# Optimization experiments

Hardware: AMD Instinct MI355X
Metric: run time of the kernel (lower is better)

Reference implementation:

```python
import jax, jax.numpy as jnp
import numpy as np

B, N_Q, N_K, DIM = 4, 4096, 4096, 256
INNER = 64
N_TOPK = 3
MINUS_INF = -1e9


def setup_inputs() -> dict:
    key = jax.random.key(0)
    ks = jax.random.split(key, 5)
    q = jax.random.normal(ks[0], (B, N_Q, DIM), dtype=jnp.float32)
    k = jax.random.normal(ks[1], (B, N_K, DIM), dtype=jnp.float32)
    v = jax.random.normal(ks[2], (B, N_K, DIM), dtype=jnp.float32)
    Wq = jax.random.normal(ks[3], (DIM, INNER), dtype=jnp.float32) * 0.02
    Wk = jax.random.normal(ks[4], (DIM, INNER), dtype=jnp.float32) * 0.02
    return {"q": q, "k": k, "v": v, "Wq": Wq, "Wk": Wk}


def reference(q, k, v, Wq, Wk):
    # v is accepted but unused, matching the torch module.
    scale = INNER ** (-0.5)  # dim_head == inner_dim == 64
    qh = (q @ Wq) * scale            # [B, N_Q, 64]
    kh = k @ Wk                      # [B, N_K, 64]
    # heads = 1 -> scores [B, 1, N_Q, N_K]
    scores = jnp.einsum('bqd,bkd->bqk', qh, kh)[:, None]
    # torch.kthvalue(k=N_K - 3) == 4th-largest value per row
    thresh = jax.lax.top_k(scores, N_TOPK + 1)[0][..., N_TOPK:N_TOPK + 1]
    masked = jnp.where(scores < thresh, MINUS_INF, scores)
    return jax.nn.softmax(masked, axis=-1)
```

## Files before the change

kernel.cpp:

```cpp
#include <hip/hip_runtime.h>
#include <hip/hip_bf16.h>
#include <math.h>

typedef float v4f __attribute__((ext_vector_type(4)));
typedef short bf16x8 __attribute__((ext_vector_type(8)));
typedef float f32x16 __attribute__((ext_vector_type(16)));

#define BATCH 4
#define NQ 4096
#define NK 4096
#define DIM 256
#define INNER 64
#define NEG_INF (-3.0e38f)
#define CAP 64

__global__ __launch_bounds__(256) void proj_kernel(
    const float* __restrict__ q, const float* __restrict__ k,
    const float* __restrict__ Wq, const float* __restrict__ Wk,
    float* __restrict__ qh, float* __restrict__ kh,
    ushort* __restrict__ qhb, ushort* __restrict__ khb)
{
  __shared__ float xs[32 * 260];
  const int bid = blockIdx.x;
  const bool isq = bid < 512;
  const float* X   = isq ? q : k;
  const float* W   = isq ? Wq : Wk;
  float*   out     = isq ? qh : kh;
  const float scale = isq ? 0.125f : 1.0f;
  const int row0 = (isq ? bid : bid - 512) * 32;
  const int t = threadIdx.x;

  #pragma unroll
  for (int it = 0; it < 8; ++it) {
    int idx = it * 256 + t;
    int r = idx >> 6, dq = idx & 63;
    v4f v = *reinterpret_cast<const v4f*>(X + (size_t)(row0 + r) * DIM + dq * 4);
    *reinterpret_cast<v4f*>(&xs[r * 260 + dq * 4]) = v;
  }
  __syncthreads();

  const int i0 = (t & 15) * 4;
  const int rg = t >> 4;
  float acc[2][4];
  #pragma unroll
  for (int p = 0; p < 2; ++p)
    #pragma unroll
    for (int i = 0; i < 4; ++i) acc[p][i] = 0.f;

  for (int d0 = 0; d0 < DIM; d0 += 4) {
    v4f w0 = *reinterpret_cast<const v4f*>(W + (d0 + 0) * INNER + i0);
    v4f w1 = *reinterpret_cast<const v4f*>(W + (d0 + 1) * INNER + i0);
    v4f w2 = *reinterpret_cast<const v4f*>(W + (d0 + 2) * INNER + i0);
    v4f w3 = *reinterpret_cast<const v4f*>(W + (d0 + 3) * INNER + i0);
    #pragma unroll
    for (int p = 0; p < 2; ++p) {
      v4f x = *reinterpret_cast<const v4f*>(&xs[(rg + 16 * p) * 260 + d0]);
      #pragma unroll
      for (int i = 0; i < 4; ++i) {
        float bs = x[0] * w0[i];
        bs = fmaf(x[1], w1[i], bs);
        bs = fmaf(x[2], w2[i], bs);
        bs = fmaf(x[3], w3[i], bs);
        acc[p][i] += bs;
      }
    }
  }

  const int d  = i0 >> 4;
  const int hi = (i0 >> 3) & 1;
  const int e0 = i0 & 7;
  #pragma unroll
  for (int p = 0; p < 2; ++p) {
    v4f o;
    ushort ob[4];
    #pragma unroll
    for (int i = 0; i < 4; ++i) {
      o[i] = acc[p][i] * scale;
      __hip_bfloat16 h = __float2bfloat16(o[i]);
      ob[i] = *reinterpret_cast<ushort*>(&h);
    }
    int rr = rg + 16 * p;
    size_t row = (size_t)(row0 + rr);
    *reinterpret_cast<v4f*>(out + row * INNER + i0) = o;
    if (isq) {
      *reinterpret_cast<uint2*>(qhb + row * INNER + i0) =
          *reinterpret_cast<uint2*>(ob);
    } else {
      size_t off = (size_t)(bid - 512) * 2048 + d * 512 + hi * 256 + rr * 8 + e0;
      *reinterpret_cast<uint2*>(khb + off) = *reinterpret_cast<uint2*>(ob);
    }
  }
}

__device__ __forceinline__ void insert5(float (&v)[5], int (&ix)[5], float x, int xi) {
  bool g0 = x > v[0], g1 = x > v[1], g2 = x > v[2], g3 = x > v[3];
  v[4]  = g3 ? v[3] : x;                 ix[4] = g3 ? ix[3] : xi;
  v[3]  = g3 ? (g2 ? v[2] : x) : v[3];   ix[3] = g3 ? (g2 ? ix[2] : xi) : ix[3];
  v[2]  = g2 ? (g1 ? v[1] : x) : v[2];   ix[2] = g2 ? (g1 ? ix[1] : xi) : ix[2];
  v[1]  = g1 ? (g0 ? v[0] : x) : v[1];   ix[1] = g1 ? (g0 ? ix[0] : xi) : ix[1];
  v[0]  = g0 ? x : v[0];                 ix[0] = g0 ? xi : ix[0];
}

__device__ __forceinline__ void insert8v(float (&v)[8], float x) {
  bool g0 = x > v[0], g1 = x > v[1], g2 = x > v[2], g3 = x > v[3];
  bool g4 = x > v[4], g5 = x > v[5], g6 = x > v[6];
  v[7] = g6 ? v[6] : x;
  v[6] = g6 ? (g5 ? v[5] : x) : v[6];
  v[5] = g5 ? (g4 ? v[4] : x) : v[5];
  v[4] = g4 ? (g3 ? v[3] : x) : v[4];
  v[3] = g3 ? (g2 ? v[2] : x) : v[3];
  v[2] = g2 ? (g1 ? v[1] : x) : v[2];
  v[1] = g1 ? (g0 ? v[0] : x) : v[1];
  v[0] = g0 ? x : v[0];
}

__global__ __launch_bounds__(512) void filter_kernel(
    const ushort* __restrict__ qhb, const ushort* __restrict__ khb,
    const float* __restrict__ qh, const float* __restrict__ kh,
    float* __restrict__ out)
{
  __shared__ float qhf[32][68];
  __shared__ float sm[32][16];
  __shared__ float tau[32];
  __shared__ int   cnt[32];
  __shared__ int   cand[32][CAP];
  __shared__ float exactv[32][CAP];
  __shared__ float w5[32][5];
  __shared__ int   id5[32][6];

  const int t   = threadIdx.x;
  const int bid = blockIdx.x;
  const int wg  = (bid & 7) * 64 + (bid >> 3);
  const int b   = wg >> 7;
  const int q0  = (wg & 127) * 32;
  const int qg  = t >> 6;
  const int kg  = t & 63;
  const int ln  = kg & 31;
  const int hi  = kg >> 5;

  float* obase = out + ((size_t)b * NQ + q0) * (size_t)NK;
  const v4f z = {0.f, 0.f, 0.f, 0.f};

  if (t < 256) {
    int row = t >> 3, c8 = (t & 7) * 8;
    const float* src = qh + ((size_t)b * NQ + q0 + row) * INNER + c8;
    *reinterpret_cast<v4f*>(&qhf[row][c8])     = *reinterpret_cast<const v4f*>(src);
    *reinterpret_cast<v4f*>(&qhf[row][c8 + 4]) = *reinterpret_cast<const v4f*>(src + 4);
  }
  if (t < 32) cnt[t] = 0;

  const ushort* qptr = qhb + ((size_t)b * NQ + q0 + ln) * INNER + hi * 8;
  bf16x8 qf0 = *reinterpret_cast<const bf16x8*>(qptr);
  bf16x8 qf1 = *reinterpret_cast<const bf16x8*>(qptr + 16);
  bf16x8 qf2 = *reinterpret_cast<const bf16x8*>(qptr + 32);
  bf16x8 qf3 = *reinterpret_cast<const bf16x8*>(qptr + 48);

  const ushort* ktile = khb + ((size_t)b * 128 + qg * 16) * 2048;

  float smax = NEG_INF;
  {
    bf16x8 n0 = *reinterpret_cast<const bf16x8*>(ktile +        kg * 8);
    bf16x8 n1 = *reinterpret_cast<const bf16x8*>(ktile +  512 + kg * 8);
    bf16x8 n2 = *reinterpret_cast<const bf16x8*>(ktile + 1024 + kg * 8);
    bf16x8 n3 = *reinterpret_cast<const bf16x8*>(ktile + 1536 + kg * 8);
    for (int t16 = 0; t16 < 16; ++t16) {
      bf16x8 k0 = n0, k1 = n1, k2 = n2, k3 = n3;
      const ushort* nb = ktile + (size_t)(t16 + 1 < 16 ? t16 + 1 : 15) * 2048;
      n0 = *reinterpret_cast<const bf16x8*>(nb +        kg * 8);
      n1 = *reinterpret_cast<const bf16x8*>(nb +  512 + kg * 8);
      n2 = *reinterpret_cast<const bf16x8*>(nb + 1024 + kg * 8);
      n3 = *reinterpret_cast<const bf16x8*>(nb + 1536 + kg * 8);

      *reinterpret_cast<v4f*>(obase + (size_t)t16 * 4096 + t * 8)     = z;
      *reinterpret_cast<v4f*>(obase + (size_t)t16 * 4096 + t * 8 + 4) = z;

      f32x16 acc = {0.f, 0.f, 0.f, 0.f, 0.f, 0.f, 0.f, 0.f,
                    0.f, 0.f, 0.f, 0.f, 0.f, 0.f, 0.f, 0.f};
      acc = __builtin_amdgcn_mfma_f32_32x32x16_bf16(k0, qf0, acc, 0, 0, 0);
      acc = __builtin_amdgcn_mfma_f32_32x32x16_bf16(k1, qf1, acc, 0, 0, 0);
      acc = __builtin_amdgcn_mfma_f32_32x32x16_bf16(k2, qf2, acc, 0, 0, 0);
      acc = __builtin_amdgcn_mfma_f32_32x32x16_bf16(k3, qf3, acc, 0, 0, 0);

      float m0 = fmaxf(fmaxf(acc[0],  acc[1]),  fmaxf(acc[2],  acc[3]));
      float m1 = fmaxf(fmaxf(acc[4],  acc[5]),  fmaxf(acc[6],  acc[7]));
      float m2 = fmaxf(fmaxf(acc[8],  acc[9]),  fmaxf(acc[10], acc[11]));
      float m3 = fmaxf(fmaxf(acc[12], acc[13]), fmaxf(acc[14], acc[15]));
      smax = fmaxf(smax, fmaxf(fmaxf(m0, m1), fmaxf(m2, m3)));
    }
  }
  sm[ln][qg * 2 + hi] = smax;
  __syncthreads();

  if (t < 32) {
    float rv[8];
    #pragma unroll
    for (int j = 0; j < 8; ++j) rv[j] = NEG_INF;
    #pragma unroll
    for (int s = 0; s < 16; ++s) {
      float x = sm[t][s];
      if (x > rv[7]) insert8v(rv, x);
    }
    tau[t] = rv[7];
  }
  __syncthreads();

  const float tl = tau[ln];
  {
    bf16x8 n0 = *reinterpret_cast<const bf16x8*>(ktile +        kg * 8);
    bf16x8 n1 = *reinterpret_cast<const bf16x8*>(ktile +  512 + kg * 8);
    bf16x8 n2 = *reinterpret_cast<const bf16x8*>(ktile + 1024 + kg * 8);
    bf16x8 n3 = *reinterpret_cast<const bf16x8*>(ktile + 1536 + kg * 8);
    for (int t16 = 0; t16 < 16; ++t16) {
      bf16x8 k0 = n0, k1 = n1, k2 = n2, k3 = n3;
      const ushort* nb = ktile + (size_t)(t16 + 1 < 16 ? t16 + 1 : 15) * 2048;
      n0 = *reinterpret_cast<const bf16x8*>(nb +        kg * 8);
      n1 = *reinterpret_cast<const bf16x8*>(nb +  512 + kg * 8);
      n2 = *reinterpret_cast<const bf16x8*>(nb + 1024 + kg * 8);
      n3 = *reinterpret_cast<const bf16x8*>(nb + 1536 + kg * 8);

      *reinterpret_cast<v4f*>(obase + (size_t)(16 + t16) * 4096 + t * 8)     = z;
      *reinterpret_cast<v4f*>(obase + (size_t)(16 + t16) * 4096 + t * 8 + 4) = z;

      f32x16 acc = {0.f, 0.f, 0.f, 0.f, 0.f, 0.f, 0.f, 0.f,
                    0.f, 0.f, 0.f, 0.f, 0.f, 0.f, 0.f, 0.f};
      acc = __builtin_amdgcn_mfma_f32_32x32x16_bf16(k0, qf0, acc, 0, 0, 0);
      acc = __builtin_amdgcn_mfma_f32_32x32x16_bf16(k1, qf1, acc, 0, 0, 0);
      acc = __builtin_amdgcn_mfma_f32_32x32x16_bf16(k2, qf2, acc, 0, 0, 0);
      acc = __builtin_amdgcn_mfma_f32_32x32x16_bf16(k3, qf3, acc, 0, 0, 0);

      const int kb0 = qg * 512 + t16 * 32 + 4 * hi;
#define CHK(r) { float x_ = acc[r]; \
                 if (x_ >= tl) { \
                   int p_ = atomicAdd(&cnt[ln], 1); \
                   if (p_ < CAP) cand[ln][p_] = kb0 + ((r) & 3) + 8 * ((r) >> 2); } }
      CHK(0)  CHK(1)  CHK(2)  CHK(3)
      CHK(4)  CHK(5)  CHK(6)  CHK(7)
      CHK(8)  CHK(9)  CHK(10) CHK(11)
      CHK(12) CHK(13) CHK(14) CHK(15)
#undef CHK
    }
  }
  __syncthreads();

  {
    int row = t >> 4, j0 = t & 15;
    int n = min(cnt[row], CAP);
    for (int jj = j0; jj < n; jj += 16) {
      int idx = cand[row][jj];
      const float* kcol = kh + ((size_t)b * NK + idx) * INNER;
      float acc = 0.f;
      #pragma unroll
      for (int dd = 0; dd < INNER; dd += 4) {
        v4f kv = *reinterpret_cast<const v4f*>(kcol + dd);
        v4f qv = *reinterpret_cast<const v4f*>(&qhf[row][dd]);
        float bs = qv[0] * kv[0];
        bs = fmaf(qv[1], kv[1], bs);
        bs = fmaf(qv[2], kv[2], bs);
        bs = fmaf(qv[3], kv[3], bs);
        acc += bs;
      }
      exactv[row][jj] = acc;
    }
  }
  __syncthreads();

  if (t < 32) {
    int n = min(cnt[t], CAP);
    float rv[5]; int ri[5];
    #pragma unroll
    for (int j = 0; j < 5; ++j) { rv[j] = NEG_INF; ri[j] = 0; }
    for (int j = 0; j < n; ++j) {
      float x = exactv[t][j];
      if (x > rv[4]) insert5(rv, ri, x, cand[t][j]);
    }
    bool inc4 = (rv[4] >= rv[3]);
    float e1 = expf(rv[1] - rv[0]);
    float e2 = expf(rv[2] - rv[0]);
    float e3 = expf(rv[3] - rv[0]);
    float e4 = inc4 ? expf(rv[4] - rv[0]) : 0.0f;
    float inv = 1.0f / (1.0f + e1 + e2 + e3 + e4);
    w5[t][0] = inv;      w5[t][1] = e1 * inv;  w5[t][2] = e2 * inv;
    w5[t][3] = e3 * inv; w5[t][4] = e4 * inv;
    #pragma unroll
    for (int j = 0; j < 5; ++j) id5[t][j] = ri[j];
    id5[t][5] = inc4 ? 5 : 4;
  }
  __syncthreads();

  if (t < 160) {
    int row = t / 5, j = t % 5;
    if (j < id5[row][5])
      obase[(size_t)row * NK + id5[row][j]] = w5[row][j];
  }
}

extern "C" void kernel_launch(void* const* d_in, const int* in_sizes, int n_in,
                              void* d_out, int out_size, void* d_ws, size_t ws_size,
                              hipStream_t stream) {
  const float* q  = (const float*)d_in[0];
  const float* k  = (const float*)d_in[1];
  const float* Wq = (const float*)d_in[3];
  const float* Wk = (const float*)d_in[4];

  const size_t NE = (size_t)BATCH * NQ * INNER;
  float*  qh  = (float*)d_ws;
  float*  kh  = qh + NE;
  ushort* qhb = (ushort*)(kh + NE);
  ushort* khb = qhb + NE;

  proj_kernel<<<1024, 256, 0, stream>>>(q, k, Wq, Wk, qh, kh, qhb, khb);
  filter_kernel<<<512, 512, 0, stream>>>(qhb, khb, qh, kh, (float*)d_out);
}
```

Measured before the change: 124.9 us.

## Split key range across two blocks per query tile and merge top-k afterward

Each query tile's key range is now split into two halves handled by separate workgroups, doubling the filter grid. Each half finds a local top-8 (value, index) per row and writes it to a workspace buffer instead of writing the softmax output directly. A new merge kernel combines the two halves into the top-5 per row, computes the softmax weights and scatters them into the zeroed output. This is meant to raise parallelism and latency hiding for the zero-fill and MFMA work, at the cost of an extra launch and a small intermediate buffer.

Measured after the change: 189.2 us. +51.4%, slower.

```diff
diff --git a/kernel.cpp b/kernel.cpp
--- a/kernel.cpp
+++ b/kernel.cpp
@@ -101,6 +101,19 @@
   v[0]  = g0 ? x : v[0];                 ix[0] = g0 ? xi : ix[0];
 }
 
+__device__ __forceinline__ void insert8(float (&v)[8], int (&ix)[8], float x, int xi) {
+  bool g0 = x > v[0], g1 = x > v[1], g2 = x > v[2], g3 = x > v[3];
+  bool g4 = x > v[4], g5 = x > v[5], g6 = x > v[6];
+  v[7] = g6 ? v[6] : x;                 ix[7] = g6 ? ix[6] : xi;
+  v[6] = g6 ? (g5 ? v[5] : x) : v[6];   ix[6] = g6 ? (g5 ? ix[5] : xi) : ix[6];
+  v[5] = g5 ? (g4 ? v[4] : x) : v[5];   ix[5] = g5 ? (g4 ? ix[4] : xi) : ix[5];
+  v[4] = g4 ? (g3 ? v[3] : x) : v[4];   ix[4] = g4 ? (g3 ? ix[3] : xi) : ix[4];
+  v[3] = g3 ? (g2 ? v[2] : x) : v[3];   ix[3] = g3 ? (g2 ? ix[2] : xi) : ix[3];
+  v[2] = g2 ? (g1 ? v[1] : x) : v[2];   ix[2] = g2 ? (g1 ? ix[1] : xi) : ix[2];
+  v[1] = g1 ? (g0 ? v[0] : x) : v[1];   ix[1] = g1 ? (g0 ? ix[0] : xi) : ix[1];
+  v[0] = g0 ? x : v[0];                 ix[0] = g0 ? xi : ix[0];
+}
+
 __device__ __forceinline__ void insert8v(float (&v)[8], float x) {
   bool g0 = x > v[0], g1 = x > v[1], g2 = x > v[2], g3 = x > v[3];
   bool g4 = x > v[4], g5 = x > v[5], g6 = x > v[6];
@@ -117,7 +130,7 @@
 __global__ __launch_bounds__(512) void filter_kernel(
     const ushort* __restrict__ qhb, const ushort* __restrict__ khb,
     const float* __restrict__ qh, const float* __restrict__ kh,
-    float* __restrict__ out)
+    float2* __restrict__ hbuf, float* __restrict__ out)
 {
   __shared__ float qhf[32][68];
   __shared__ float sm[32][16];
@@ -125,20 +138,20 @@
   __shared__ int   cnt[32];
   __shared__ int   cand[32][CAP];
   __shared__ float exactv[32][CAP];
-  __shared__ float w5[32][5];
-  __shared__ int   id5[32][6];
 
   const int t   = threadIdx.x;
   const int bid = blockIdx.x;
-  const int wg  = (bid & 7) * 64 + (bid >> 3);
-  const int b   = wg >> 7;
-  const int q0  = (wg & 127) * 32;
+  const int wg  = (bid & 7) * 128 + (bid >> 3);
+  const int b    = wg >> 8;
+  const int rr   = wg & 255;
+  const int q0   = (rr >> 1) * 32;
+  const int half = rr & 1;
   const int qg  = t >> 6;
   const int kg  = t & 63;
   const int ln  = kg & 31;
   const int hi  = kg >> 5;
 
-  float* obase = out + ((size_t)b * NQ + q0) * (size_t)NK;
+  float* zbase = out + ((size_t)b * NQ + q0 + half * 16) * (size_t)NK;
   const v4f z = {0.f, 0.f, 0.f, 0.f};
 
   if (t < 256) {
@@ -155,7 +168,8 @@
   bf16x8 qf2 = *reinterpret_cast<const bf16x8*>(qptr + 32);
   bf16x8 qf3 = *reinterpret_cast<const bf16x8*>(qptr + 48);
 
-  const ushort* ktile = khb + ((size_t)b * 128 + qg * 16) * 2048;
+  const int tile0 = half * 64 + qg * 8;
+  const ushort* ktile = khb + ((size_t)b * 128 + tile0) * 2048;
 
   float smax = NEG_INF;
   {
@@ -163,16 +177,16 @@
     bf16x8 n1 = *reinterpret_cast<const bf16x8*>(ktile +  512 + kg * 8);
     bf16x8 n2 = *reinterpret_cast<const bf16x8*>(ktile + 1024 + kg * 8);
     bf16x8 n3 = *reinterpret_cast<const bf16x8*>(ktile + 1536 + kg * 8);
-    for (int t16 = 0; t16 < 16; ++t16) {
+    for (int t8 = 0; t8 < 8; ++t8) {
       bf16x8 k0 = n0, k1 = n1, k2 = n2, k3 = n3;
-      const ushort* nb = ktile + (size_t)(t16 + 1 < 16 ? t16 + 1 : 15) * 2048;
+      const ushort* nb = ktile + (size_t)(t8 + 1 < 8 ? t8 + 1 : 7) * 2048;
       n0 = *reinterpret_cast<const bf16x8*>(nb +        kg * 8);
       n1 = *reinterpret_cast<const bf16x8*>(nb +  512 + kg * 8);
       n2 = *reinterpret_cast<const bf16x8*>(nb + 1024 + kg * 8);
       n3 = *reinterpret_cast<const bf16x8*>(nb + 1536 + kg * 8);
 
-      *reinterpret_cast<v4f*>(obase + (size_t)t16 * 4096 + t * 8)     = z;
-      *reinterpret_cast<v4f*>(obase + (size_t)t16 * 4096 + t * 8 + 4) = z;
+      *reinterpret_cast<v4f*>(zbase + (size_t)t8 * 4096 + t * 8)     = z;
+      *reinterpret_cast<v4f*>(zbase + (size_t)t8 * 4096 + t * 8 + 4) = z;
 
       f32x16 acc = {0.f, 0.f, 0.f, 0.f, 0.f, 0.f, 0.f, 0.f,
                     0.f, 0.f, 0.f, 0.f, 0.f, 0.f, 0.f, 0.f};
@@ -210,16 +224,16 @@
     bf16x8 n1 = *reinterpret_cast<const bf16x8*>(ktile +  512 + kg * 8);
     bf16x8 n2 = *reinterpret_cast<const bf16x8*>(ktile + 1024 + kg * 8);
     bf16x8 n3 = *reinterpret_cast<const bf16x8*>(ktile + 1536 + kg * 8);
-    for (int t16 = 0; t16 < 16; ++t16) {
+    for (int t8 = 0; t8 < 8; ++t8) {
       bf16x8 k0 = n0, k1 = n1, k2 = n2, k3 = n3;
-      const ushort* nb = ktile + (size_t)(t16 + 1 < 16 ? t16 + 1 : 15) * 2048;
+      const ushort* nb = ktile + (size_t)(t8 + 1 < 8 ? t8 + 1 : 7) * 2048;
       n0 = *reinterpret_cast<const bf16x8*>(nb +        kg * 8);
       n1 = *reinterpret_cast<const bf16x8*>(nb +  512 + kg * 8);
       n2 = *reinterpret_cast<const bf16x8*>(nb + 1024 + kg * 8);
       n3 = *reinterpret_cast<const bf16x8*>(nb + 1536 + kg * 8);
 
-      *reinterpret_cast<v4f*>(obase + (size_t)(16 + t16) * 4096 + t * 8)     = z;
-      *reinterpret_cast<v4f*>(obase + (size_t)(16 + t16) * 4096 + t * 8 + 4) = z;
+      *reinterpret_cast<v4f*>(zbase + (size_t)(8 + t8) * 4096 + t * 8)     = z;
+      *reinterpret_cast<v4f*>(zbase + (size_t)(8 + t8) * 4096 + t * 8 + 4) = z;
 
       f32x16 acc = {0.f, 0.f, 0.f, 0.f, 0.f, 0.f, 0.f, 0.f,
                     0.f, 0.f, 0.f, 0.f, 0.f, 0.f, 0.f, 0.f};
@@ -228,7 +242,7 @@
       acc = __builtin_amdgcn_mfma_f32_32x32x16_bf16(k2, qf2, acc, 0, 0, 0);
       acc = __builtin_amdgcn_mfma_f32_32x32x16_bf16(k3, qf3, acc, 0, 0, 0);
 
-      const int kb0 = qg * 512 + t16 * 32 + 4 * hi;
+      const int kb0 = tile0 * 32 + t8 * 32 + 4 * hi;
 #define CHK(r) { float x_ = acc[r]; \
                  if (x_ >= tl) { \
                    int p_ = atomicAdd(&cnt[ln], 1); \
@@ -266,32 +280,50 @@
 
   if (t < 32) {
     int n = min(cnt[t], CAP);
-    float rv[5]; int ri[5];
-    #pragma unroll
-    for (int j = 0; j < 5; ++j) { rv[j] = NEG_INF; ri[j] = 0; }
+    float rv[8]; int ri[8];
+    #pragma unroll
+    for (int j = 0; j < 8; ++j) { rv[j] = NEG_INF; ri[j] = 0; }
     for (int j = 0; j < n; ++j) {
       float x = exactv[t][j];
-      if (x > rv[4]) insert5(rv, ri, x, cand[t][j]);
-    }
-    bool inc4 = (rv[4] >= rv[3]);
-    float e1 = expf(rv[1] - rv[0]);
-    float e2 = expf(rv[2] - rv[0]);
-    float e3 = expf(rv[3] - rv[0]);
-    float e4 = inc4 ? expf(rv[4] - rv[0]) : 0.0f;
-    float inv = 1.0f / (1.0f + e1 + e2 + e3 + e4);
-    w5[t][0] = inv;      w5[t][1] = e1 * inv;  w5[t][2] = e2 * inv;
-    w5[t][3] = e3 * inv; w5[t][4] = e4 * inv;
-    #pragma unroll
-    for (int j = 0; j < 5; ++j) id5[t][j] = ri[j];
-    id5[t][5] = inc4 ? 5 : 4;
-  }
-  __syncthreads();
-
-  if (t < 160) {
-    int row = t / 5, j = t % 5;
-    if (j < id5[row][5])
-      obase[(size_t)row * NK + id5[row][j]] = w5[row][j];
-  }
+      if (x > rv[7]) insert8(rv, ri, x, cand[t][j]);
+    }
+    size_t grow = (size_t)b * NQ + q0 + t;
+    float2* hp = hbuf + (grow * 2 + half) * 8;
+    #pragma unroll
+    for (int j = 0; j < 8; ++j) {
+      float2 e; e.x = rv[j]; e.y = __int_as_float(ri[j]);
+      hp[j] = e;
+    }
+  }
+}
+
+__global__ __launch_bounds__(256) void merge_kernel(
+    const float2* __restrict__ hbuf, float* __restrict__ out)
+{
+  int row = blockIdx.x * 256 + threadIdx.x;
+  const float2* hp = hbuf + (size_t)row * 16;
+  float rv[5]; int ri[5];
+  #pragma unroll
+  for (int j = 0; j < 5; ++j) { rv[j] = NEG_INF; ri[j] = 0; }
+  #pragma unroll
+  for (int j = 0; j < 16; ++j) {
+    float2 e = hp[j];
+    if (e.x > rv[4]) insert5(rv, ri, e.x, __float_as_int(e.y));
+  }
+  bool inc4 = (rv[4] >= rv[3]);
+  float e1 = expf(rv[1] - rv[0]);
+  float e2 = expf(rv[2] - rv[0]);
+  float e3 = expf(rv[3] - rv[0]);
+  float e4 = inc4 ? expf(rv[4] - rv[0]) : 0.0f;
+  float inv = 1.0f / (1.0f + e1 + e2 + e3 + e4);
+  float w0 = inv, w1 = e1 * inv, w2 = e2 * inv, w3 = e3 * inv, w4 = e4 * inv;
+
+  float* op = out + (size_t)row * NK;
+  op[ri[0]] = w0;
+  op[ri[1]] = w1;
+  op[ri[2]] = w2;
+  op[ri[3]] = w3;
+  if (inc4) op[ri[4]] = w4;
 }
 
 extern "C" void kernel_launch(void* const* d_in, const int* in_sizes, int n_in,
@@ -303,11 +335,13 @@
   const float* Wk = (const float*)d_in[4];
 
   const size_t NE = (size_t)BATCH * NQ * INNER;
-  float*  qh  = (float*)d_ws;
-  float*  kh  = qh + NE;
-  ushort* qhb = (ushort*)(kh + NE);
-  ushort* khb = qhb + NE;
+  float*  qh   = (float*)d_ws;
+  float*  kh   = qh + NE;
+  ushort* qhb  = (ushort*)(kh + NE);
+  ushort* khb  = qhb + NE;
+  float2* hbuf = (float2*)(khb + NE);
 
   proj_kernel<<<1024, 256, 0, stream>>>(q, k, Wq, Wk, qh, kh, qhb, khb);
-  filter_kernel<<<512, 512, 0, stream>>>(qhb, khb, qh, kh, (float*)d_out);
-}
+  filter_kernel<<<1024, 512, 0, stream>>>(qhb, khb, qh, kh, hbuf, (float*)d_out);
+  merge_kernel<<<BATCH * NQ / 256, 256, 0, stream>>>(hbuf, (float*)d_out);
+}
```
